# Kernel optimization log

Measured on AMD Instinct MI355X. Metric: run time of the kernel, lower is better.

Reference implementation:

```python
import jax, jax.numpy as jnp
import numpy as np

B, T = 64, 512
DC = 256   # dim_concept
DR = 256   # dim_correct
DL = 256   # dim_latent
DA = 256   # dim_attention
NC = 1024  # num_concept


def setup_inputs() -> dict:
    key = jax.random.key(0)
    ks = jax.random.split(key, 12)
    s = 0.05
    inp = {
        'concept_seq': jax.random.randint(ks[0], (B, T), 0, NC, dtype=jnp.int32),
        'correct_seq': jax.random.randint(ks[1], (B, T), 0, 2, dtype=jnp.int32),
        'embed_concept': jax.random.normal(ks[2], (NC, DC), jnp.float32) * s,
        'embed_correct': jax.random.normal(ks[3], (2, DR), jnp.float32) * s,
        'W_ih': jax.random.normal(ks[4], (4 * DL, DC + DR), jnp.float32) * s,
        'W_hh': jax.random.normal(ks[5], (4 * DL, DL), jnp.float32) * s,
        'b_ih': jax.random.normal(ks[6], (4 * DL,), jnp.float32) * s,
        'b_hh': jax.random.normal(ks[7], (4 * DL,), jnp.float32) * s,
        'mlp_W': jax.random.normal(ks[8], (DA, DL), jnp.float32) * s,
        'mlp_b': jnp.zeros((DA,), jnp.float32),
        'sim_W': jax.random.normal(ks[9], (1, DA), jnp.float32) * s,
        'fc_W': jax.random.normal(ks[10], (NC, 2 * DL), jnp.float32) * s,
        'fc_b': jnp.zeros((NC,), jnp.float32),
    }
    return inp


def _lstm(x, W_ih, W_hh, b_ih, b_hh):
    # x: [B, T, D] -> hs: [B, T, H]; PyTorch gate order i, f, g, o
    Bsz = x.shape[0]
    H = W_hh.shape[1]
    xg = jnp.einsum('btd,gd->btg', x, W_ih) + b_ih + b_hh  # precompute input gates

    def step(carry, xt):
        h, c = carry
        gates = xt + h @ W_hh.T
        i, f, g, o = jnp.split(gates, 4, axis=-1)
        i = jax.nn.sigmoid(i)
        f = jax.nn.sigmoid(f)
        g = jnp.tanh(g)
        o = jax.nn.sigmoid(o)
        c = f * c + i * g
        h = o * jnp.tanh(c)
        return (h, c), h

    init = (jnp.zeros((Bsz, H), x.dtype), jnp.zeros((Bsz, H), x.dtype))
    _, hs = jax.lax.scan(step, init, xg.transpose(1, 0, 2))
    return hs.transpose(1, 0, 2)


def _forward(concept_seq, correct_seq, embed_concept, embed_correct,
             W_ih, W_hh, b_ih, b_hh, mlp_W, mlp_b, sim_W, fc_W, fc_b):
    concept_emb = embed_concept[concept_seq]          # [B,T,DC]
    correct_emb = embed_correct[correct_seq]          # [B,T,DR]
    cc = jnp.concatenate([concept_emb, correct_emb], axis=2)
    rc = jnp.concatenate([correct_emb, concept_emb], axis=2)
    sel = (correct_seq == 1)[:, :, None]
    interaction_emb = jnp.where(sel, cc, rc)          # [B,T,DC+DR]

    lstm_out = _lstm(interaction_emb, W_ih, W_hh, b_ih, b_hh)  # [B,T,DL]

    # attention: per-position scalar score, broadcast to causal BxTxT
    att = jnp.tanh(jnp.einsum('btd,ad->bta', lstm_out, mlp_W) + mlp_b)
    score = jnp.einsum('bta,oa->bto', att, sim_W)[..., 0]      # [B,T]
    seq = lstm_out.shape[1]
    upper = jnp.triu(jnp.ones((seq, seq), bool), k=1)          # mask j > i
    logits = jnp.where(upper[None], -jnp.inf, score[:, None, :])
    alphas = jax.nn.softmax(logits, axis=-1)                   # [B,T,T]
    attn_out = jnp.einsum('bij,bjd->bid', alphas, lstm_out)    # [B,T,DL]
    attn_excl = jnp.cumsum(attn_out, axis=1) - attn_out        # exclusive cumsum
    final = jnp.concatenate([attn_excl, lstm_out], axis=2)     # [B,T,2*DL]

    logits_out = jnp.einsum('btd,cd->btc', final, fc_W) + fc_b
    return jax.nn.sigmoid(logits_out)                          # [B,T,NC]


def reference(concept_seq, correct_seq, embed_concept, embed_correct,
              W_ih, W_hh, b_ih, b_hh, mlp_W, mlp_b, sim_W, fc_W, fc_b):
    return _forward(concept_seq, correct_seq, embed_concept, embed_correct,
                    W_ih, W_hh, b_ih, b_hh, mlp_W, mlp_b, sim_W, fc_W, fc_b)
```

## Files before the change

kernel.cpp:

```cpp
#include <hip/hip_runtime.h>


typedef __attribute__((ext_vector_type(4))) float f32x4;
typedef __attribute__((ext_vector_type(8))) short s16x8;
typedef __attribute__((ext_vector_type(4))) short s16x4;

__device__ __forceinline__ unsigned short f2b(float f) {
  unsigned u = __float_as_uint(f);
  u += 0x7FFFu + ((u >> 16) & 1u);
  return (unsigned short)(u >> 16);
}
__device__ __forceinline__ float b2f(unsigned short s) {
  return __uint_as_float(((unsigned)s) << 16);
}
__device__ __forceinline__ float sigf(float x) {
  return __builtin_amdgcn_rcpf(1.f + __expf(-x));
}
__device__ __forceinline__ float tanhf_(float x) {
  return 1.f - 2.f * __builtin_amdgcn_rcpf(1.f + __expf(2.f * x));
}

__global__ void prep_kernel(const float* __restrict__ W_ih,
                            const float* __restrict__ fc_W,
                            const float* __restrict__ mlp_W,
                            unsigned short* __restrict__ wihb,
                            unsigned short* __restrict__ fcwb,
                            unsigned short* __restrict__ mlpwb,
                            unsigned short* __restrict__ fcw1lo,
                            int* __restrict__ flags) {
  int i = blockIdx.x * 256 + threadIdx.x;
  if (i < 524288) {
    wihb[i] = f2b(W_ih[i]);
  } else if (i < 1048576) {
    int j = i - 524288;
    float w = fc_W[j];
    unsigned short h = f2b(w);
    fcwb[j] = h;
    int col = j & 511;
    if (col < 256) fcw1lo[(size_t)(j >> 9) * 256 + col] = f2b(w - b2f(h));
  } else if (i < 1114112) {
    mlpwb[i - 1048576] = f2b(mlp_W[i - 1048576]);
  }
  if (i < 1024) flags[i] = 0;
}

__global__ void interact_kernel(const int* __restrict__ cseq,
                                const int* __restrict__ kseq,
                                const float* __restrict__ embC,
                                const float* __restrict__ embR,
                                unsigned short* __restrict__ inter) {
  int bt = blockIdx.x * 4 + (threadIdx.x >> 6);
  int l = threadIdx.x & 63;
  int c = cseq[bt], k = kseq[bt];
  const float* h1 = k ? (embC + (size_t)c * 256) : embR;
  const float* h2 = k ? (embR + 256) : (embC + (size_t)c * 256);
  int seg = l * 8;
  const float* src = (seg < 256) ? (h1 + seg) : (h2 + (seg - 256));
  s16x8 vv;
#pragma unroll
  for (int q = 0; q < 8; ++q) vv[q] = (short)f2b(src[q]);
  *(s16x8*)(inter + (size_t)bt * 512 + seg) = vv;
}

__global__ __launch_bounds__(256, 2) void gemm_xg(
    const unsigned short* __restrict__ A, const unsigned short* __restrict__ W,
    const float* __restrict__ bias1, const float* __restrict__ bias2,
    float* __restrict__ outp) {
  constexpr int KW = 512;
  __shared__ char smem[20480];
  char* As = smem;
  char* Ws = smem + 10240;
  const int tn = blockIdx.x, tm = blockIdx.y;
  const int tid = threadIdx.x;
  const int v = tid >> 6, l = tid & 63;
  const int wm = v >> 1, wn = v & 1;
  const int lr = l & 15, lh = l >> 4;

  f32x4 acc[4][4];
#pragma unroll
  for (int i = 0; i < 4; ++i)
#pragma unroll
    for (int jj = 0; jj < 4; ++jj) acc[i][jj] = f32x4{0.f, 0.f, 0.f, 0.f};

  const unsigned short* Ag = A + (size_t)(tm * 128) * KW;
  const unsigned short* Wg = W + (size_t)(tn * 128) * KW;

  s16x8 ra[2], rw[2];
#pragma unroll
  for (int q = 0; q < 2; ++q) {
    int slot = q * 256 + tid, row = slot >> 2, c16 = slot & 3;
    ra[q] = *(const s16x8*)(Ag + (size_t)row * KW + c16 * 8);
    rw[q] = *(const s16x8*)(Wg + (size_t)row * KW + c16 * 8);
  }
  for (int kk = 0; kk < KW / 32; ++kk) {
#pragma unroll
    for (int q = 0; q < 2; ++q) {
      int slot = q * 256 + tid, row = slot >> 2, c16 = slot & 3;
      *(s16x8*)(As + row * 80 + c16 * 16) = ra[q];
      *(s16x8*)(Ws + row * 80 + c16 * 16) = rw[q];
    }
    __syncthreads();
    if (kk + 1 < KW / 32) {
#pragma unroll
      for (int q = 0; q < 2; ++q) {
        int slot = q * 256 + tid, row = slot >> 2, c16 = slot & 3;
        ra[q] = *(const s16x8*)(Ag + (size_t)row * KW + (kk + 1) * 32 + c16 * 8);
        rw[q] = *(const s16x8*)(Wg + (size_t)row * KW + (kk + 1) * 32 + c16 * 8);
      }
    }
    s16x8 af[4], wf[4];
#pragma unroll
    for (int mt = 0; mt < 4; ++mt) {
      int r = wm * 64 + mt * 16 + lr;
      af[mt] = *(const s16x8*)(As + r * 80 + lh * 16);
    }
#pragma unroll
    for (int nt = 0; nt < 4; ++nt) {
      int n = wn * 64 + nt * 16 + lr;
      wf[nt] = *(const s16x8*)(Ws + n * 80 + lh * 16);
    }
#pragma unroll
    for (int mt = 0; mt < 4; ++mt)
#pragma unroll
      for (int nt = 0; nt < 4; ++nt)
        acc[mt][nt] =
            __builtin_amdgcn_mfma_f32_16x16x32_bf16(af[mt], wf[nt], acc[mt][nt], 0, 0, 0);
    __syncthreads();
  }
#pragma unroll
  for (int mt = 0; mt < 4; ++mt) {
#pragma unroll
    for (int nt = 0; nt < 4; ++nt) {
      int col = tn * 128 + wn * 64 + nt * 16 + lr;
      float bv = bias1[col] + bias2[col];
#pragma unroll
      for (int vi = 0; vi < 4; ++vi) {
        int row = tm * 128 + wm * 64 + mt * 16 + lh * 4 + vi;
        outp[(size_t)row * 1024 + col] = acc[mt][nt][vi] + bv;
      }
    }
  }
}

__global__ __launch_bounds__(256, 1) void lstm_kernel(
    const float* __restrict__ W_hh, const float* __restrict__ xg,
    unsigned short* __restrict__ hbuf_hi, unsigned short* __restrict__ hbuf_lo,
    unsigned short* __restrict__ lstm_out, int* __restrict__ flags) {
  const int w = blockIdx.x, tid = threadIdx.x;
  const int g = w >> 2, j = w & 3;
  const int v = tid >> 6, l = tid & 63;
  const int ww = (w << 2) | v;
  const int lr = l & 15, lh = l >> 4;

  s16x8 wf[4][8];
#pragma unroll
  for (int gt = 0; gt < 4; ++gt) {
    const float* wr = W_hh + (size_t)(gt * 256 + j * 64 + v * 16 + lr) * 256;
#pragma unroll
    for (int kc = 0; kc < 8; ++kc) {
      const float* p = wr + kc * 32 + lh * 8;
      s16x8 t;
#pragma unroll
      for (int q = 0; q < 8; ++q) t[q] = (short)f2b(p[q]);
      wf[gt][kc] = t;
    }
  }
  const int bcol = g * 16 + lr;
  const int dbase = j * 64 + v * 16 + lh * 4;
  const float* xgp = xg + (size_t)bcol * 512 * 1024 + dbase;
  float cst[4] = {0.f, 0.f, 0.f, 0.f};

  f32x4 xpre[4];
#pragma unroll
  for (int gt = 0; gt < 4; ++gt) xpre[gt] = *(const f32x4*)(xgp + gt * 256);

  for (int t = 0; t < 512; ++t) {
    f32x4 acc[4];
#pragma unroll
    for (int gt = 0; gt < 4; ++gt) acc[gt] = xpre[gt];
    if (t > 0) {
      int* f = flags + l * 16;
      while (1) {
        int fv = __hip_atomic_load(f, __ATOMIC_ACQUIRE, __HIP_MEMORY_SCOPE_AGENT);
        if (__all(fv >= t)) break;
        __builtin_amdgcn_s_sleep(1);
      }
      size_t hb_off = ((size_t)(((t - 1) & 1) * 4 + g) * 16 + lr) * 256;
      s16x8 hf_hi[8], hf_lo[8];
#pragma unroll
      for (int kc = 0; kc < 8; ++kc) {
        hf_hi[kc] = *(const s16x8*)(hbuf_hi + hb_off + kc * 32 + lh * 8);
        hf_lo[kc] = *(const s16x8*)(hbuf_lo + hb_off + kc * 32 + lh * 8);
      }
#pragma unroll
      for (int gt = 0; gt < 4; ++gt) {
#pragma unroll
        for (int kc = 0; kc < 8; ++kc)
          acc[gt] = __builtin_amdgcn_mfma_f32_16x16x32_bf16(wf[gt][kc], hf_hi[kc],
                                                            acc[gt], 0, 0, 0);
#pragma unroll
        for (int kc = 0; kc < 8; ++kc)
          acc[gt] = __builtin_amdgcn_mfma_f32_16x16x32_bf16(wf[gt][kc], hf_lo[kc],
                                                            acc[gt], 0, 0, 0);
      }
    }
    if (t < 511) {
#pragma unroll
      for (int gt = 0; gt < 4; ++gt)
        xpre[gt] = *(const f32x4*)(xgp + (size_t)(t + 1) * 1024 + gt * 256);
    }
    s16x4 hhi, hlo;
#pragma unroll
    for (int vi = 0; vi < 4; ++vi) {
      float ig = sigf(acc[0][vi]);
      float fg = sigf(acc[1][vi]);
      float gg = tanhf_(acc[2][vi]);
      float og = sigf(acc[3][vi]);
      cst[vi] = fg * cst[vi] + ig * gg;
      float hv = og * tanhf_(cst[vi]);
      unsigned short hb = f2b(hv);
      hhi[vi] = (short)hb;
      hlo[vi] = (short)f2b(hv - b2f(hb));
    }
    size_t wo = ((size_t)((t & 1) * 4 + g) * 16 + lr) * 256 + dbase;
    *(s16x4*)(hbuf_hi + wo) = hhi;
    *(s16x4*)(hbuf_lo + wo) = hlo;
    *(s16x4*)(lstm_out + ((size_t)bcol * 512 + t) * 256 + dbase) = hhi;
    if (l == 0)
      __hip_atomic_store(flags + ww * 16, t + 1, __ATOMIC_RELEASE,
                         __HIP_MEMORY_SCOPE_AGENT);
  }
}

__global__ __launch_bounds__(512, 1) void score_kernel(
    const unsigned short* __restrict__ A,
    const unsigned short* __restrict__ W,
    const float* __restrict__ mlp_b, const float* __restrict__ sim_W,
    float* __restrict__ score) {
  __shared__ char smem[32768];
  char* As = smem;
  char* Ws = smem + 10240;
  float* part = (float*)(smem + 30720);
  const int tm = blockIdx.x, tid = threadIdx.x;
  const int v = tid >> 6, l = tid & 63;
  const int wm = v >> 2, wn = v & 3;
  const int lr = l & 15, lh = l >> 4;

  f32x4 acc[4][4];
#pragma unroll
  for (int i = 0; i < 4; ++i)
#pragma unroll
    for (int jj = 0; jj < 4; ++jj) acc[i][jj] = f32x4{0.f, 0.f, 0.f, 0.f};

  const unsigned short* Ag = A + (size_t)(tm * 128) * 256;
  s16x8 ra, rw[2];
  {
    int slot = tid, row = slot >> 2, c16 = slot & 3;
    ra = *(const s16x8*)(Ag + (size_t)row * 256 + c16 * 8);
  }
#pragma unroll
  for (int q = 0; q < 2; ++q) {
    int slot = q * 512 + tid, row = slot >> 2, c16 = slot & 3;
    rw[q] = *(const s16x8*)(W + (size_t)row * 256 + c16 * 8);
  }
  for (int kk = 0; kk < 8; ++kk) {
    {
      int slot = tid, row = slot >> 2, c16 = slot & 3;
      *(s16x8*)(As + row * 80 + c16 * 16) = ra;
    }
#pragma unroll
    for (int q = 0; q < 2; ++q) {
      int slot = q * 512 + tid, row = slot >> 2, c16 = slot & 3;
      *(s16x8*)(Ws + row * 80 + c16 * 16) = rw[q];
    }
    __syncthreads();
    if (kk < 7) {
      {
        int slot = tid, row = slot >> 2, c16 = slot & 3;
        ra = *(const s16x8*)(Ag + (size_t)row * 256 + (kk + 1) * 32 + c16 * 8);
      }
#pragma unroll
      for (int q = 0; q < 2; ++q) {
        int slot = q * 512 + tid, row = slot >> 2, c16 = slot & 3;
        rw[q] = *(const s16x8*)(W + (size_t)row * 256 + (kk + 1) * 32 + c16 * 8);
      }
    }
    s16x8 af[4], wfr[4];
#pragma unroll
    for (int mt = 0; mt < 4; ++mt) {
      int r = wm * 64 + mt * 16 + lr;
      af[mt] = *(const s16x8*)(As + r * 80 + lh * 16);
    }
#pragma unroll
    for (int nt = 0; nt < 4; ++nt) {
      int n = wn * 64 + nt * 16 + lr;
      wfr[nt] = *(const s16x8*)(Ws + n * 80 + lh * 16);
    }
#pragma unroll
    for (int mt = 0; mt < 4; ++mt)
#pragma unroll
      for (int nt = 0; nt < 4; ++nt)
        acc[mt][nt] =
            __builtin_amdgcn_mfma_f32_16x16x32_bf16(af[mt], wfr[nt], acc[mt][nt], 0, 0, 0);
    __syncthreads();
  }
  float rowsum[4][4];
#pragma unroll
  for (int mt = 0; mt < 4; ++mt)
#pragma unroll
    for (int vi = 0; vi < 4; ++vi) rowsum[mt][vi] = 0.f;
#pragma unroll
  for (int nt = 0; nt < 4; ++nt) {
    int n = wn * 64 + nt * 16 + lr;
    float mb = mlp_b[n], sw = sim_W[n];
#pragma unroll
    for (int mt = 0; mt < 4; ++mt)
#pragma unroll
      for (int vi = 0; vi < 4; ++vi)
        rowsum[mt][vi] += tanhf_(acc[mt][nt][vi] + mb) * sw;
  }
#pragma unroll
  for (int mt = 0; mt < 4; ++mt)
#pragma unroll
    for (int vi = 0; vi < 4; ++vi) {
#pragma unroll
      for (int off = 1; off < 16; off <<= 1)
        rowsum[mt][vi] += __shfl_xor(rowsum[mt][vi], off, 64);
    }
  if (lr == 0) {
#pragma unroll
    for (int mt = 0; mt < 4; ++mt)
#pragma unroll
      for (int vi = 0; vi < 4; ++vi)
        part[wn * 128 + wm * 64 + mt * 16 + lh * 4 + vi] = rowsum[mt][vi];
  }
  __syncthreads();
  if (tid < 128) {
    float s = part[tid] + part[128 + tid] + part[256 + tid] + part[384 + tid];
    score[tm * 128 + tid] = s;
  }
}

__global__ __launch_bounds__(256, 1) void attn_kernel(
    const float* __restrict__ score, const unsigned short* __restrict__ lstm_out,
    unsigned short* __restrict__ attno) {
  __shared__ float e_s[512];
  __shared__ float rden_s[512];
  const int b = blockIdx.x, tid = threadIdx.x;
  if (tid < 64) {
    float sv[8];
    float m = -1e30f;
    const float* sp = score + b * 512 + tid * 8;
#pragma unroll
    for (int q = 0; q < 8; ++q) {
      sv[q] = sp[q];
      m = fmaxf(m, sv[q]);
    }
#pragma unroll
    for (int off = 1; off < 64; off <<= 1) m = fmaxf(m, __shfl_xor(m, off, 64));
    float loc[8];
    float sum = 0.f;
#pragma unroll
    for (int q = 0; q < 8; ++q) {
      loc[q] = __expf(sv[q] - m);
      sum += loc[q];
    }
    float incl = sum;
#pragma unroll
    for (int d2 = 1; d2 < 64; d2 <<= 1) {
      float o = __shfl_up(incl, d2, 64);
      if (tid >= d2) incl += o;
    }
    float run = incl - sum;
#pragma unroll
    for (int q = 0; q < 8; ++q) {
      run += loc[q];
      e_s[tid * 8 + q] = loc[q];
      rden_s[tid * 8 + q] = __builtin_amdgcn_rcpf(run);
    }
  }
  __syncthreads();
  const int d = tid;
  float num = 0.f;
  const unsigned short* hp = lstm_out + (size_t)b * 512 * 256 + d;
  unsigned short* ap = attno + (size_t)b * 512 * 256 + d;
  for (int t = 0; t < 512; ++t) {
    num += e_s[t] * b2f(hp[(size_t)t * 256]);
    ap[(size_t)t * 256] = f2b(num * rden_s[t]);
  }
}

__global__ __launch_bounds__(256, 2) void gemm_fc(
    const unsigned short* __restrict__ A1,
    const unsigned short* __restrict__ A2,
    const unsigned short* __restrict__ W,
    const unsigned short* __restrict__ W1lo,
    const float* __restrict__ bias, float* __restrict__ pout,
    float* __restrict__ qout) {
  __shared__ char smem[20480];
  char* As = smem;
  char* Ws = smem + 10240;
  const int tn = blockIdx.x, tm = blockIdx.y;
  const int tid = threadIdx.x;
  const int v = tid >> 6, l = tid & 63;
  const int wm = v >> 1, wn = v & 1;
  const int lr = l & 15, lh = l >> 4;

  f32x4 acc[4][4];
#pragma unroll
  for (int i = 0; i < 4; ++i)
#pragma unroll
    for (int jj = 0; jj < 4; ++jj) acc[i][jj] = f32x4{0.f, 0.f, 0.f, 0.f};

  auto aload = [&](int kk, int slot) -> s16x8 {
    int row = tm * 128 + (slot >> 2);
    int c = (slot & 3) * 8;
    if (kk < 16) return *(const s16x8*)(A1 + (size_t)row * 256 + (kk & 7) * 32 + c);
    return *(const s16x8*)(A2 + (size_t)row * 256 + ((kk - 16) & 7) * 32 + c);
  };
  auto wload = [&](int kk, int slot) -> s16x8 {
    int row = tn * 128 + (slot >> 2);
    int c = (slot & 3) * 8;
    if (kk < 8) return *(const s16x8*)(W + (size_t)row * 512 + kk * 32 + c);
    if (kk < 16)
      return *(const s16x8*)(W1lo + (size_t)row * 256 + (kk - 8) * 32 + c);
    return *(const s16x8*)(W + (size_t)row * 512 + 256 + (kk - 16) * 32 + c);
  };

  s16x8 ra[2], rw[2];
#pragma unroll
  for (int q = 0; q < 2; ++q) {
    ra[q] = aload(0, q * 256 + tid);
    rw[q] = wload(0, q * 256 + tid);
  }
  for (int kk = 0; kk < 24; ++kk) {
#pragma unroll
    for (int q = 0; q < 2; ++q) {
      int slot = q * 256 + tid, row = slot >> 2, c16 = slot & 3;
      *(s16x8*)(As + row * 80 + c16 * 16) = ra[q];
      *(s16x8*)(Ws + row * 80 + c16 * 16) = rw[q];
    }
    __syncthreads();
    if (kk + 1 < 24) {
#pragma unroll
      for (int q = 0; q < 2; ++q) {
        ra[q] = aload(kk + 1, q * 256 + tid);
        rw[q] = wload(kk + 1, q * 256 + tid);
      }
    }
    s16x8 af[4], wfr[4];
#pragma unroll
    for (int mt = 0; mt < 4; ++mt) {
      int r = wm * 64 + mt * 16 + lr;
      af[mt] = *(const s16x8*)(As + r * 80 + lh * 16);
    }
#pragma unroll
    for (int nt = 0; nt < 4; ++nt) {
      int n = wn * 64 + nt * 16 + lr;
      wfr[nt] = *(const s16x8*)(Ws + n * 80 + lh * 16);
    }
#pragma unroll
    for (int mt = 0; mt < 4; ++mt)
#pragma unroll
      for (int nt = 0; nt < 4; ++nt)
        acc[mt][nt] =
            __builtin_amdgcn_mfma_f32_16x16x32_bf16(af[mt], wfr[nt], acc[mt][nt], 0, 0, 0);
    __syncthreads();
    if (kk == 15) {
#pragma unroll
      for (int mt = 0; mt < 4; ++mt) {
#pragma unroll
        for (int nt = 0; nt < 4; ++nt) {
          int col = tn * 128 + wn * 64 + nt * 16 + lr;
#pragma unroll
          for (int vi = 0; vi < 4; ++vi) {
            int row = tm * 128 + wm * 64 + mt * 16 + lh * 4 + vi;
            pout[(size_t)row * 1024 + col] = acc[mt][nt][vi];
          }
          acc[mt][nt] = f32x4{0.f, 0.f, 0.f, 0.f};
        }
      }
    }
  }
#pragma unroll
  for (int mt = 0; mt < 4; ++mt) {
#pragma unroll
    for (int nt = 0; nt < 4; ++nt) {
      int col = tn * 128 + wn * 64 + nt * 16 + lr;
      float bv = bias[col];
#pragma unroll
      for (int vi = 0; vi < 4; ++vi) {
        int row = tm * 128 + wm * 64 + mt * 16 + lh * 4 + vi;
        qout[(size_t)row * 1024 + col] = acc[mt][nt][vi] + bv;
      }
    }
  }
}

__global__ __launch_bounds__(256, 1) void scan_pq(const float* __restrict__ p,
                                                  float* __restrict__ q) {
  const int c = blockIdx.x * 256 + threadIdx.x;
  const int b = blockIdx.y;
  const size_t base = ((size_t)b * 512) * 1024 + c;
  float cum = 0.f;
#pragma unroll 4
  for (int t = 0; t < 512; ++t) {
    size_t idx = base + (size_t)t * 1024;
    float pv = p[idx];
    float qv = q[idx];
    q[idx] = sigf(qv + cum);
    cum += pv;
  }
}

extern "C" void kernel_launch(void* const* d_in, const int* in_sizes, int n_in,
                              void* d_out, int out_size, void* d_ws, size_t ws_size,
                              hipStream_t stream) {
  const int* cseq = (const int*)d_in[0];
  const int* kseq = (const int*)d_in[1];
  const float* embC = (const float*)d_in[2];
  const float* embR = (const float*)d_in[3];
  const float* W_ih = (const float*)d_in[4];
  const float* W_hh = (const float*)d_in[5];
  const float* b_ih = (const float*)d_in[6];
  const float* b_hh = (const float*)d_in[7];
  const float* mlp_W = (const float*)d_in[8];
  const float* mlp_b = (const float*)d_in[9];
  const float* sim_W = (const float*)d_in[10];
  const float* fc_W = (const float*)d_in[11];
  const float* fc_b = (const float*)d_in[12];
  char* ws = (char*)d_ws;

  unsigned short* inter  = (unsigned short*)(ws + 0);
  unsigned short* wihb   = (unsigned short*)(ws + 33554432);
  unsigned short* fcwb   = (unsigned short*)(ws + 34603008);
  unsigned short* mlpwb  = (unsigned short*)(ws + 35651584);
  unsigned short* fcw1lo = (unsigned short*)(ws + 35782656);
  float* xg              = (float*)(ws + 36306944);
  float* pbuf            = xg;
  unsigned short* lstm   = (unsigned short*)(ws + 170524672);
  unsigned short* attno  = (unsigned short*)(ws + 187301888);
  unsigned short* hbuf_hi= (unsigned short*)(ws + 204079104);
  unsigned short* hbuf_lo= (unsigned short*)(ws + 204144640);
  int* flags             = (int*)(ws + 204210176);
  float* score           = (float*)(ws + 204214272);

  float* qbuf = (float*)d_out;

  prep_kernel<<<dim3(4352), dim3(256), 0, stream>>>(W_ih, fc_W, mlp_W, wihb,
                                                    fcwb, mlpwb, fcw1lo, flags);
  interact_kernel<<<dim3(8192), dim3(256), 0, stream>>>(cseq, kseq, embC, embR,
                                                        inter);
  gemm_xg<<<dim3(8, 256), dim3(256), 0, stream>>>(inter, wihb, b_ih, b_hh, xg);
  lstm_kernel<<<dim3(16), dim3(256), 0, stream>>>(W_hh, xg, hbuf_hi, hbuf_lo,
                                                  lstm, flags);
  score_kernel<<<dim3(256), dim3(512), 0, stream>>>(lstm, mlpwb, mlp_b, sim_W,
                                                    score);
  attn_kernel<<<dim3(64), dim3(256), 0, stream>>>(score, lstm, attno);
  gemm_fc<<<dim3(8, 256), dim3(256), 0, stream>>>(attno, lstm, fcwb, fcw1lo,
                                                  fc_b, pbuf, qbuf);
  scan_pq<<<dim3(4, 64), dim3(256), 0, stream>>>(pbuf, qbuf);
}
```

Measured before the change: 3.929 ms.

## Co-locate LSTM batch-group blocks on one XCD and use lighter sync

```diff
diff --git a/kernel.cpp b/kernel.cpp
--- a/kernel.cpp
+++ b/kernel.cpp
@@ -41,7 +41,7 @@
   } else if (i < 1114112) {
     mlpwb[i - 1048576] = f2b(mlp_W[i - 1048576]);
   }
-  if (i < 1024) flags[i] = 0;
+  if (i < 1536) flags[i] = 0;
 }
 
 __global__ void interact_kernel(const int* __restrict__ cseq,
@@ -146,11 +146,37 @@
     const float* __restrict__ W_hh, const float* __restrict__ xg,
     unsigned short* __restrict__ hbuf_hi, unsigned short* __restrict__ hbuf_lo,
     unsigned short* __restrict__ lstm_out, int* __restrict__ flags) {
-  const int w = blockIdx.x, tid = threadIdx.x;
-  const int g = w >> 2, j = w & 3;
+  const int blk = blockIdx.x;
+  const int gg = blk & 7;
+  if (gg >= 4) return;
+  const int g = gg;
+  const int j = blk >> 3;
+  const int tid = threadIdx.x;
   const int v = tid >> 6, l = tid & 63;
-  const int ww = (w << 2) | v;
   const int lr = l & 15, lh = l >> 4;
+
+  __shared__ int sh_fast;
+  if (tid == 0) {
+    int xcd;
+    asm volatile("s_getreg_b32 %0, hwreg(HW_REG_XCC_ID)" : "=s"(xcd));
+    xcd &= 15;
+    __hip_atomic_store(flags + 1024 + (g * 4 + j) * 16, xcd + 1,
+                       __ATOMIC_RELEASE, __HIP_MEMORY_SCOPE_AGENT);
+    int ok = 1, id0 = 0;
+    for (int s2 = 0; s2 < 4; ++s2) {
+      int v2;
+      do {
+        v2 = __hip_atomic_load(flags + 1024 + (g * 4 + s2) * 16,
+                               __ATOMIC_ACQUIRE, __HIP_MEMORY_SCOPE_AGENT);
+        if (v2 == 0) __builtin_amdgcn_s_sleep(1);
+      } while (v2 == 0);
+      if (s2 == 0) id0 = v2;
+      else if (v2 != id0) ok = 0;
+    }
+    sh_fast = ok;
+  }
+  __syncthreads();
+  const bool fast = (sh_fast != 0);
 
   s16x8 wf[4][8];
 #pragma unroll
@@ -169,66 +195,169 @@
   const int dbase = j * 64 + v * 16 + lh * 4;
   const float* xgp = xg + (size_t)bcol * 512 * 1024 + dbase;
   float cst[4] = {0.f, 0.f, 0.f, 0.f};
+  int* myflag = flags + (g * 16 + j * 4 + v) * 16;
+  int* fp = flags + (g * 16 + (l & 15)) * 16;
 
   f32x4 xpre[4];
 #pragma unroll
   for (int gt = 0; gt < 4; ++gt) xpre[gt] = *(const f32x4*)(xgp + gt * 256);
 
-  for (int t = 0; t < 512; ++t) {
-    f32x4 acc[4];
-#pragma unroll
-    for (int gt = 0; gt < 4; ++gt) acc[gt] = xpre[gt];
-    if (t > 0) {
-      int* f = flags + l * 16;
-      while (1) {
-        int fv = __hip_atomic_load(f, __ATOMIC_ACQUIRE, __HIP_MEMORY_SCOPE_AGENT);
-        if (__all(fv >= t)) break;
-        __builtin_amdgcn_s_sleep(1);
-      }
-      size_t hb_off = ((size_t)(((t - 1) & 1) * 4 + g) * 16 + lr) * 256;
-      s16x8 hf_hi[8], hf_lo[8];
-#pragma unroll
-      for (int kc = 0; kc < 8; ++kc) {
-        hf_hi[kc] = *(const s16x8*)(hbuf_hi + hb_off + kc * 32 + lh * 8);
-        hf_lo[kc] = *(const s16x8*)(hbuf_lo + hb_off + kc * 32 + lh * 8);
-      }
-#pragma unroll
-      for (int gt = 0; gt < 4; ++gt) {
-#pragma unroll
-        for (int kc = 0; kc < 8; ++kc)
-          acc[gt] = __builtin_amdgcn_mfma_f32_16x16x32_bf16(wf[gt][kc], hf_hi[kc],
-                                                            acc[gt], 0, 0, 0);
-#pragma unroll
-        for (int kc = 0; kc < 8; ++kc)
-          acc[gt] = __builtin_amdgcn_mfma_f32_16x16x32_bf16(wf[gt][kc], hf_lo[kc],
-                                                            acc[gt], 0, 0, 0);
-      }
-    }
-    if (t < 511) {
-#pragma unroll
-      for (int gt = 0; gt < 4; ++gt)
-        xpre[gt] = *(const f32x4*)(xgp + (size_t)(t + 1) * 1024 + gt * 256);
-    }
-    s16x4 hhi, hlo;
-#pragma unroll
-    for (int vi = 0; vi < 4; ++vi) {
-      float ig = sigf(acc[0][vi]);
-      float fg = sigf(acc[1][vi]);
-      float gg = tanhf_(acc[2][vi]);
-      float og = sigf(acc[3][vi]);
-      cst[vi] = fg * cst[vi] + ig * gg;
-      float hv = og * tanhf_(cst[vi]);
-      unsigned short hb = f2b(hv);
-      hhi[vi] = (short)hb;
-      hlo[vi] = (short)f2b(hv - b2f(hb));
-    }
-    size_t wo = ((size_t)((t & 1) * 4 + g) * 16 + lr) * 256 + dbase;
-    *(s16x4*)(hbuf_hi + wo) = hhi;
-    *(s16x4*)(hbuf_lo + wo) = hlo;
-    *(s16x4*)(lstm_out + ((size_t)bcol * 512 + t) * 256 + dbase) = hhi;
-    if (l == 0)
-      __hip_atomic_store(flags + ww * 16, t + 1, __ATOMIC_RELEASE,
-                         __HIP_MEMORY_SCOPE_AGENT);
+  if (fast) {
+    int slowpoll = 0;
+    for (int t = 0; t < 512; ++t) {
+      f32x4 acc[4];
+#pragma unroll
+      for (int gt = 0; gt < 4; ++gt) acc[gt] = xpre[gt];
+      if (t > 0) {
+        if (!slowpoll) {
+          int spins = 0;
+          while (true) {
+            int fv;
+            asm volatile(
+                "global_load_dword %0, %1, off sc0\n\ts_waitcnt vmcnt(0)"
+                : "=v"(fv)
+                : "v"(fp)
+                : "memory");
+            if (__all(fv >= t)) break;
+            if (++spins > 4096) { slowpoll = 1; break; }
+          }
+        }
+        if (slowpoll) {
+          while (true) {
+            int fv = __hip_atomic_load(fp, __ATOMIC_ACQUIRE,
+                                       __HIP_MEMORY_SCOPE_AGENT);
+            if (__all(fv >= t)) break;
+            __builtin_amdgcn_s_sleep(1);
+          }
+        }
+        __builtin_amdgcn_sched_barrier(0);
+        size_t hb_off = ((size_t)(((t - 1) & 1) * 4 + g) * 16 + lr) * 256;
+        s16x8 hf_hi[8], hf_lo[8];
+#pragma unroll
+        for (int kc = 0; kc < 8; ++kc) {
+          asm volatile("global_load_dwordx4 %0, %1, off sc0"
+                       : "=v"(hf_hi[kc])
+                       : "v"(hbuf_hi + hb_off + kc * 32 + lh * 8));
+          asm volatile("global_load_dwordx4 %0, %1, off sc0"
+                       : "=v"(hf_lo[kc])
+                       : "v"(hbuf_lo + hb_off + kc * 32 + lh * 8));
+        }
+        {
+          const float* xa = xgp + (size_t)((t < 511) ? t + 1 : t) * 1024;
+#pragma unroll
+          for (int gt = 0; gt < 4; ++gt)
+            asm volatile("global_load_dwordx4 %0, %1, off"
+                         : "=v"(xpre[gt])
+                         : "v"(xa + gt * 256));
+        }
+        asm volatile("s_waitcnt vmcnt(4)" ::: "memory");
+        __builtin_amdgcn_sched_barrier(0);
+#pragma unroll
+        for (int gt = 0; gt < 4; ++gt) {
+#pragma unroll
+          for (int kc = 0; kc < 8; ++kc)
+            acc[gt] = __builtin_amdgcn_mfma_f32_16x16x32_bf16(
+                wf[gt][kc], hf_hi[kc], acc[gt], 0, 0, 0);
+#pragma unroll
+          for (int kc = 0; kc < 8; ++kc)
+            acc[gt] = __builtin_amdgcn_mfma_f32_16x16x32_bf16(
+                wf[gt][kc], hf_lo[kc], acc[gt], 0, 0, 0);
+        }
+      } else {
+        const float* xa = xgp + 1024;
+#pragma unroll
+        for (int gt = 0; gt < 4; ++gt)
+          asm volatile("global_load_dwordx4 %0, %1, off"
+                       : "=v"(xpre[gt])
+                       : "v"(xa + gt * 256));
+      }
+      s16x4 hhi, hlo;
+#pragma unroll
+      for (int vi = 0; vi < 4; ++vi) {
+        float ig = sigf(acc[0][vi]);
+        float fg = sigf(acc[1][vi]);
+        float gb = tanhf_(acc[2][vi]);
+        float og = sigf(acc[3][vi]);
+        cst[vi] = fg * cst[vi] + ig * gb;
+        float hv = og * tanhf_(cst[vi]);
+        unsigned short hb = f2b(hv);
+        hhi[vi] = (short)hb;
+        hlo[vi] = (short)f2b(hv - b2f(hb));
+      }
+      size_t wo = ((size_t)((t & 1) * 4 + g) * 16 + lr) * 256 + dbase;
+      asm volatile("global_store_dwordx2 %0, %1, off sc0" ::"v"(hbuf_hi + wo),
+                   "v"(hhi)
+                   : "memory");
+      asm volatile("global_store_dwordx2 %0, %1, off sc0" ::"v"(hbuf_lo + wo),
+                   "v"(hlo)
+                   : "memory");
+      *(s16x4*)(lstm_out + ((size_t)bcol * 512 + t) * 256 + dbase) = hhi;
+      asm volatile("s_waitcnt vmcnt(0)" ::: "memory");
+      if (l == 0) {
+        int tv = t + 1;
+        asm volatile("global_store_dword %0, %1, off sc0" ::"v"(myflag),
+                     "v"(tv)
+                     : "memory");
+      }
+      __builtin_amdgcn_sched_barrier(0);
+    }
+  } else {
+    for (int t = 0; t < 512; ++t) {
+      f32x4 acc[4];
+#pragma unroll
+      for (int gt = 0; gt < 4; ++gt) acc[gt] = xpre[gt];
+      if (t > 0) {
+        while (true) {
+          int fv =
+              __hip_atomic_load(fp, __ATOMIC_ACQUIRE, __HIP_MEMORY_SCOPE_AGENT);
+          if (__all(fv >= t)) break;
+          __builtin_amdgcn_s_sleep(1);
+        }
+        size_t hb_off = ((size_t)(((t - 1) & 1) * 4 + g) * 16 + lr) * 256;
+        s16x8 hf_hi[8], hf_lo[8];
+#pragma unroll
+        for (int kc = 0; kc < 8; ++kc) {
+          hf_hi[kc] = *(const s16x8*)(hbuf_hi + hb_off + kc * 32 + lh * 8);
+          hf_lo[kc] = *(const s16x8*)(hbuf_lo + hb_off + kc * 32 + lh * 8);
+        }
+#pragma unroll
+        for (int gt = 0; gt < 4; ++gt) {
+#pragma unroll
+          for (int kc = 0; kc < 8; ++kc)
+            acc[gt] = __builtin_amdgcn_mfma_f32_16x16x32_bf16(
+                wf[gt][kc], hf_hi[kc], acc[gt], 0, 0, 0);
+#pragma unroll
+          for (int kc = 0; kc < 8; ++kc)
+            acc[gt] = __builtin_amdgcn_mfma_f32_16x16x32_bf16(
+                wf[gt][kc], hf_lo[kc], acc[gt], 0, 0, 0);
+        }
+      }
+      if (t < 511) {
+#pragma unroll
+        for (int gt = 0; gt < 4; ++gt)
+          xpre[gt] = *(const f32x4*)(xgp + (size_t)(t + 1) * 1024 + gt * 256);
+      }
+      s16x4 hhi, hlo;
+#pragma unroll
+      for (int vi = 0; vi < 4; ++vi) {
+        float ig = sigf(acc[0][vi]);
+        float fg = sigf(acc[1][vi]);
+        float gb = tanhf_(acc[2][vi]);
+        float og = sigf(acc[3][vi]);
+        cst[vi] = fg * cst[vi] + ig * gb;
+        float hv = og * tanhf_(cst[vi]);
+        unsigned short hb = f2b(hv);
+        hhi[vi] = (short)hb;
+        hlo[vi] = (short)f2b(hv - b2f(hb));
+      }
+      size_t wo = ((size_t)((t & 1) * 4 + g) * 16 + lr) * 256 + dbase;
+      *(s16x4*)(hbuf_hi + wo) = hhi;
+      *(s16x4*)(hbuf_lo + wo) = hlo;
+      *(s16x4*)(lstm_out + ((size_t)bcol * 512 + t) * 256 + dbase) = hhi;
+      if (l == 0)
+        __hip_atomic_store(myflag, t + 1, __ATOMIC_RELEASE,
+                           __HIP_MEMORY_SCOPE_AGENT);
+    }
   }
 }
 
@@ -543,7 +672,7 @@
   unsigned short* hbuf_hi= (unsigned short*)(ws + 204079104);
   unsigned short* hbuf_lo= (unsigned short*)(ws + 204144640);
   int* flags             = (int*)(ws + 204210176);
-  float* score           = (float*)(ws + 204214272);
+  float* score           = (float*)(ws + 204218368);
 
   float* qbuf = (float*)d_out;
 
@@ -552,7 +681,7 @@
   interact_kernel<<<dim3(8192), dim3(256), 0, stream>>>(cseq, kseq, embC, embR,
                                                         inter);
   gemm_xg<<<dim3(8, 256), dim3(256), 0, stream>>>(inter, wihb, b_ih, b_hh, xg);
-  lstm_kernel<<<dim3(16), dim3(256), 0, stream>>>(W_hh, xg, hbuf_hi, hbuf_lo,
+  lstm_kernel<<<dim3(32), dim3(256), 0, stream>>>(W_hh, xg, hbuf_hi, hbuf_lo,
                                                   lstm, flags);
   score_kernel<<<dim3(256), dim3(512), 0, stream>>>(lstm, mlpwb, mlp_b, sim_W,
                                                     score);
```

New measurement: 3.448 ms. 12.2% less time.
